# Optimization experiments

Hardware: AMD Instinct MI355X
Metric: run time of the kernel (lower is better)

The kernel has to match this reference:

```python
import jax, jax.numpy as jnp
import numpy as np

B, T, C, H, D = 2048, 64, 64, 8, 64  # batch, block_size, n_embed, num_heads, head_size


def setup_inputs() -> dict:
    key = jax.random.key(0)
    ks = jax.random.split(key, 6)
    s = C ** -0.5  # approx torch Linear init scale
    x = jax.random.normal(ks[0], (B, T, C), dtype=jnp.float32)
    Wq = jax.random.uniform(ks[1], (H, C, D), jnp.float32, -s, s)  # per-head query weights (in, out)
    Wk = jax.random.uniform(ks[2], (H, C, D), jnp.float32, -s, s)
    Wv = jax.random.uniform(ks[3], (H, C, D), jnp.float32, -s, s)
    sp = (H * D) ** -0.5
    Wproj = jax.random.uniform(ks[4], (H * D, C), jnp.float32, -sp, sp)  # proj weight (in, out)
    bproj = jax.random.uniform(ks[5], (C,), jnp.float32, -sp, sp)
    return {"x": x, "Wq": Wq, "Wk": Wk, "Wv": Wv, "Wproj": Wproj, "bproj": bproj}


def reference(x, Wq, Wk, Wv, Wproj, bproj):
    # per-head projections, vectorized over heads (original loops over Head modules)
    q = jnp.einsum('btc,hcd->bhtd', x, Wq)
    k = jnp.einsum('btc,hcd->bhtd', x, Wk)
    v = jnp.einsum('btc,hcd->bhtd', x, Wv)
    scores = jnp.einsum('bhtd,bhsd->bhts', q, k) * (D ** -0.5)  # [B,H,T,T]
    causal = jnp.tril(jnp.ones((T, T), dtype=bool))
    scores = jnp.where(causal, scores, jnp.float32(-jnp.inf))
    wei = jax.nn.softmax(scores, axis=-1)  # dropout = identity in eval mode
    out = jnp.einsum('bhts,bhsd->bhtd', wei, v)
    out = out.transpose(0, 2, 1, 3).reshape(B, T, H * D)  # concat heads on last dim
    out = out @ Wproj + bproj  # output projection (dropout = identity in eval)
    return out
```

## Files before the change

### kernel.cpp

```cpp
#include <hip/hip_runtime.h>

typedef __bf16 bf16x8 __attribute__((ext_vector_type(8)));
typedef float f32x4 __attribute__((ext_vector_type(4)));
typedef unsigned short u16x4 __attribute__((ext_vector_type(4)));
typedef unsigned int u32x4 __attribute__((ext_vector_type(4)));

#define LDA 72

__device__ __forceinline__ unsigned short f2bf(float f) {
  __bf16 b = (__bf16)f;
  return __builtin_bit_cast(unsigned short, b);
}

__device__ __forceinline__ u16x4 pack4(f32x4 v) {
  u16x4 r;
  r[0] = f2bf(v[0]); r[1] = f2bf(v[1]); r[2] = f2bf(v[2]); r[3] = f2bf(v[3]);
  return r;
}

__device__ __forceinline__ bf16x8 frag8(const unsigned short* p) {
  typedef unsigned short u16x8v __attribute__((ext_vector_type(8)));
  return __builtin_bit_cast(bf16x8, *reinterpret_cast<const u16x8v*>(p));
}

#define MFMA(a, b, c) __builtin_amdgcn_mfma_f32_16x16x32_bf16(a, b, c, 0, 0, 0)

__device__ __forceinline__ void cfrag2bfrag(const f32x4 v[4], bf16x8 out[2]) {
  unsigned O[4][2];
  #pragma unroll
  for (int si = 0; si < 4; ++si) {
    u16x4 p = pack4(v[si]);
    O[si][0] = (unsigned)p[0] | ((unsigned)p[1] << 16);
    O[si][1] = (unsigned)p[2] | ((unsigned)p[3] << 16);
  }
  unsigned H[2][2][2];
  #pragma unroll
  for (int s1 = 0; s1 < 2; ++s1)
    #pragma unroll
    for (int d = 0; d < 2; ++d) {
      auto r = __builtin_amdgcn_permlane32_swap(O[2 * s1][d], O[2 * s1 + 1][d], false, false);
      H[s1][0][d] = r[0];
      H[s1][1][d] = r[1];
    }
  #pragma unroll
  for (int e1 = 0; e1 < 2; ++e1) {
    auto r0 = __builtin_amdgcn_permlane16_swap(H[e1][0][0], H[e1][1][0], false, false);
    auto r1 = __builtin_amdgcn_permlane16_swap(H[e1][0][1], H[e1][1][1], false, false);
    u32x4 f;
    f[0] = r0[0]; f[1] = r1[0]; f[2] = r0[1]; f[3] = r1[1];
    out[e1] = __builtin_bit_cast(bf16x8, f);
  }
}

__global__ __launch_bounds__(256) void fuse_pack(
    const float* __restrict__ Wq, const float* __restrict__ Wk,
    const float* __restrict__ Wv, const float* __restrict__ Wp,
    unsigned short* __restrict__ wf) {
  __shared__ float A[64 * 65];
  __shared__ float B[64 * 65];
  const int blk = blockIdx.x;
  const int t = blk >> 3, h = blk & 7;
  const int tid = threadIdx.x;
  const float* Asrc = (t ? Wv : Wq) + h * 4096;
  const float* Bsrc = (t ? Wp : Wk) + h * 4096;
  for (int i = tid; i < 4096; i += 256) {
    A[(i >> 6) * 65 + (i & 63)] = Asrc[i];
    B[(i >> 6) * 65 + (i & 63)] = Bsrc[i];
  }
  __syncthreads();
  unsigned short* dst = wf + blk * 4096;
  for (int o = 0; o < 16; ++o) {
    int idx = o * 256 + tid;
    int k = idx >> 6, n = idx & 63;
    float s = 0.f;
    if (t == 0) {
      for (int d = 0; d < 64; ++d) s += A[k * 65 + d] * B[n * 65 + d];
      s *= 0.18033688f;
    } else {
      for (int d = 0; d < 64; ++d) s += A[k * 65 + d] * B[d * 65 + n];
    }
    int kk = k >> 5, i = k & 7, lg = (k >> 3) & 3, si = n >> 4, l15 = n & 15;
    dst[((kk * 4 + si) * 64 + lg * 16 + l15) * 8 + i] = f2bf(s);
  }
}

__global__ __launch_bounds__(256, 2) void mha_fwd(
    const float* __restrict__ x, const unsigned short* __restrict__ wf,
    const float* __restrict__ bproj, float* __restrict__ out) {
  __shared__ __attribute__((aligned(16))) unsigned short Xs[4][64 * LDA];

  const int tid  = threadIdx.x;
  const int lane = tid & 63;
  const int w    = tid >> 6;
  const int l15  = lane & 15;
  const int g    = lane >> 4;
  const int kcol = 8 * g;

  const float* xb = x + (size_t)blockIdx.x * 16384;
  #pragma unroll
  for (int it = 0; it < 16; ++it) {
    int idx = it * 1024 + tid * 4;
    float4 v = *reinterpret_cast<const float4*>(xb + idx);
    f32x4 vv = {v.x, v.y, v.z, v.w};
    int bt = idx >> 12, rem = idx & 4095;
    *reinterpret_cast<u16x4*>(&Xs[bt][(rem >> 6) * LDA + (rem & 63)]) = pack4(vv);
  }
  __syncthreads();

  bf16x8 xf[2][4];
  #pragma unroll
  for (int cc = 0; cc < 2; ++cc)
    #pragma unroll
    for (int t = 0; t < 4; ++t)
      xf[cc][t] = frag8(&Xs[w][(t * 16 + l15) * LDA + cc * 32 + kcol]);

  f32x4 oacc[4][4];
  #pragma unroll
  for (int nt = 0; nt < 4; ++nt) {
    float bias = bproj[nt * 16 + l15];
    f32x4 bv = {bias, bias, bias, bias};
    #pragma unroll
    for (int mt = 0; mt < 4; ++mt) oacc[mt][nt] = bv;
  }

  for (int h = 0; h < 8; ++h) {
    const unsigned short* mf = wf + h * 4096;
    const unsigned short* nf = wf + 32768 + h * 4096;

    bf16x8 gB[2][4];
    #pragma unroll
    for (int mt = 0; mt < 4; ++mt) {
      f32x4 gc[4] = {};
      #pragma unroll
      for (int kk = 0; kk < 2; ++kk)
        #pragma unroll
        for (int ct = 0; ct < 4; ++ct)
          gc[ct] = MFMA(frag8(&mf[(kk * 4 + ct) * 512 + lane * 8]), xf[kk][mt], gc[ct]);
      bf16x8 o2[2];
      cfrag2bfrag(gc, o2);
      gB[0][mt] = o2[0]; gB[1][mt] = o2[1];
    }

    bf16x8 pA[2][4];
    #pragma unroll
    for (int mt = 0; mt < 4; ++mt) {
      f32x4 sc[4] = {};
      #pragma unroll
      for (int cc = 0; cc < 2; ++cc)
        #pragma unroll
        for (int st = 0; st < 4; ++st)
          sc[st] = MFMA(xf[cc][st], gB[cc][mt], sc[st]);
      const int m = mt * 16 + l15;
      float sum = 0.f;
      #pragma unroll
      for (int st = 0; st < 4; ++st)
        #pragma unroll
        for (int r = 0; r < 4; ++r) {
          int s = st * 16 + 4 * g + r;
          float e = (s <= m) ? exp2f(sc[st][r]) : 0.f;
          sc[st][r] = e;
          sum += e;
        }
      sum += __shfl_xor(sum, 16);
      sum += __shfl_xor(sum, 32);
      float rinv = __builtin_amdgcn_rcpf(sum);
      #pragma unroll
      for (int st = 0; st < 4; ++st) sc[st] *= rinv;
      bf16x8 o2[2];
      cfrag2bfrag(sc, o2);
      pA[0][mt] = o2[0]; pA[1][mt] = o2[1];
    }

    bf16x8 zB[2][4];
    #pragma unroll
    for (int nt = 0; nt < 4; ++nt) {
      bf16x8 nf0 = frag8(&nf[(0 * 4 + nt) * 512 + lane * 8]);
      bf16x8 nf1 = frag8(&nf[(1 * 4 + nt) * 512 + lane * 8]);
      f32x4 zc[4] = {};
      #pragma unroll
      for (int st = 0; st < 4; ++st) {
        zc[st] = MFMA(xf[0][st], nf0, zc[st]);
        zc[st] = MFMA(xf[1][st], nf1, zc[st]);
      }
      bf16x8 o2[2];
      cfrag2bfrag(zc, o2);
      zB[0][nt] = o2[0]; zB[1][nt] = o2[1];
    }

    #pragma unroll
    for (int mt = 0; mt < 4; ++mt)
      #pragma unroll
      for (int nt = 0; nt < 4; ++nt) {
        oacc[mt][nt] = MFMA(pA[0][mt], zB[0][nt], oacc[mt][nt]);
        oacc[mt][nt] = MFMA(pA[1][mt], zB[1][nt], oacc[mt][nt]);
      }
  }

  float* ob = out + ((size_t)blockIdx.x * 4 + w) * 4096;
  #pragma unroll
  for (int mt = 0; mt < 4; ++mt)
    #pragma unroll
    for (int r = 0; r < 4; ++r) {
      float* orow = ob + (mt * 16 + 4 * g + r) * 64;
      #pragma unroll
      for (int nt = 0; nt < 4; ++nt)
        orow[nt * 16 + l15] = oacc[mt][nt][r];
    }
}

extern "C" void kernel_launch(void* const* d_in, const int* in_sizes, int n_in,
                              void* d_out, int out_size, void* d_ws, size_t ws_size,
                              hipStream_t stream) {
  const float* x  = (const float*)d_in[0];
  const float* Wq = (const float*)d_in[1];
  const float* Wk = (const float*)d_in[2];
  const float* Wv = (const float*)d_in[3];
  const float* Wp = (const float*)d_in[4];
  const float* bp = (const float*)d_in[5];
  unsigned short* wf = (unsigned short*)d_ws;

  fuse_pack<<<dim3(16), dim3(256), 0, stream>>>(Wq, Wk, Wv, Wp, wf);
  mha_fwd<<<dim3(512), dim3(256), 0, stream>>>(x, wf, bp, (float*)d_out);
}
```

Measured before the change: 61.43 us.

## Split each batch across two waves with balanced causal row tiles and skip masked MFMAs

Each wave now owns two of the four query row tiles of one batch element instead of a whole batch element. The pairs are (0,3) and (1,2) so causal work is balanced between the two waves. Score MFMAs, exp work and P·V MFMAs for fully masked key tiles are skipped at compile time via templated tile indices. The grid doubles, launch bounds ask for 4 blocks per CU, and register pressure per wave drops. The cost is that the Z (V·Wproj) fragment is now recomputed by both waves sharing a batch element.

```diff
diff --git a/kernel.cpp b/kernel.cpp
--- a/kernel.cpp
+++ b/kernel.cpp
@@ -6,6 +6,8 @@
 typedef unsigned int u32x4 __attribute__((ext_vector_type(4)));
 
 #define LDA 72
+
+template <int N> struct Int { static constexpr int value = N; };
 
 __device__ __forceinline__ unsigned short f2bf(float f) {
   __bf16 b = (__bf16)f;
@@ -84,26 +86,28 @@
   }
 }
 
-__global__ __launch_bounds__(256, 2) void mha_fwd(
+__global__ __launch_bounds__(256, 4) void mha_fwd(
     const float* __restrict__ x, const unsigned short* __restrict__ wf,
     const float* __restrict__ bproj, float* __restrict__ out) {
-  __shared__ __attribute__((aligned(16))) unsigned short Xs[4][64 * LDA];
+  __shared__ __attribute__((aligned(16))) unsigned short Xs[2][64 * LDA];
 
   const int tid  = threadIdx.x;
   const int lane = tid & 63;
   const int w    = tid >> 6;
+  const int bt   = w >> 1;
+  const int mg   = w & 1;
   const int l15  = lane & 15;
   const int g    = lane >> 4;
   const int kcol = 8 * g;
 
-  const float* xb = x + (size_t)blockIdx.x * 16384;
-  #pragma unroll
-  for (int it = 0; it < 16; ++it) {
+  const float* xb = x + (size_t)blockIdx.x * 8192;
+  #pragma unroll
+  for (int it = 0; it < 8; ++it) {
     int idx = it * 1024 + tid * 4;
     float4 v = *reinterpret_cast<const float4*>(xb + idx);
     f32x4 vv = {v.x, v.y, v.z, v.w};
-    int bt = idx >> 12, rem = idx & 4095;
-    *reinterpret_cast<u16x4*>(&Xs[bt][(rem >> 6) * LDA + (rem & 63)]) = pack4(vv);
+    int sb = idx >> 12, rem = idx & 4095;
+    *reinterpret_cast<u16x4*>(&Xs[sb][(rem >> 6) * LDA + (rem & 63)]) = pack4(vv);
   }
   __syncthreads();
 
@@ -112,100 +116,112 @@
   for (int cc = 0; cc < 2; ++cc)
     #pragma unroll
     for (int t = 0; t < 4; ++t)
-      xf[cc][t] = frag8(&Xs[w][(t * 16 + l15) * LDA + cc * 32 + kcol]);
-
-  f32x4 oacc[4][4];
+      xf[cc][t] = frag8(&Xs[bt][(t * 16 + l15) * LDA + cc * 32 + kcol]);
+
+  f32x4 oacc[2][4];
   #pragma unroll
   for (int nt = 0; nt < 4; ++nt) {
     float bias = bproj[nt * 16 + l15];
     f32x4 bv = {bias, bias, bias, bias};
-    #pragma unroll
-    for (int mt = 0; mt < 4; ++mt) oacc[mt][nt] = bv;
-  }
-
+    oacc[0][nt] = bv;
+    oacc[1][nt] = bv;
+  }
+
+  #pragma unroll 1
   for (int h = 0; h < 8; ++h) {
     const unsigned short* mf = wf + h * 4096;
     const unsigned short* nf = wf + 32768 + h * 4096;
 
-    bf16x8 gB[2][4];
-    #pragma unroll
-    for (int mt = 0; mt < 4; ++mt) {
-      f32x4 gc[4] = {};
-      #pragma unroll
-      for (int kk = 0; kk < 2; ++kk)
-        #pragma unroll
-        for (int ct = 0; ct < 4; ++ct)
-          gc[ct] = MFMA(frag8(&mf[(kk * 4 + ct) * 512 + lane * 8]), xf[kk][mt], gc[ct]);
-      bf16x8 o2[2];
-      cfrag2bfrag(gc, o2);
-      gB[0][mt] = o2[0]; gB[1][mt] = o2[1];
-    }
-
-    bf16x8 pA[2][4];
-    #pragma unroll
-    for (int mt = 0; mt < 4; ++mt) {
-      f32x4 sc[4] = {};
-      #pragma unroll
-      for (int cc = 0; cc < 2; ++cc)
+    auto head_body = [&](auto MT0C, auto MT1C) {
+      constexpr int MT0 = decltype(MT0C)::value;
+      constexpr int MT1 = decltype(MT1C)::value;
+      bf16x8 pA[2][2];
+
+      auto gs = [&](auto MTC, int lmt) {
+        constexpr int MT = decltype(MTC)::value;
+        f32x4 gc[4] = {};
+        #pragma unroll
+        for (int kk = 0; kk < 2; ++kk)
+          #pragma unroll
+          for (int ct = 0; ct < 4; ++ct)
+            gc[ct] = MFMA(frag8(&mf[(kk * 4 + ct) * 512 + lane * 8]), xf[kk][MT], gc[ct]);
+        bf16x8 gB[2];
+        cfrag2bfrag(gc, gB);
+
+        f32x4 sc[4] = {};
+        #pragma unroll
+        for (int cc = 0; cc < 2; ++cc)
+          #pragma unroll
+          for (int st = 0; st < 4; ++st)
+            if (st <= MT)
+              sc[st] = MFMA(xf[cc][st], gB[cc], sc[st]);
+
+        const int m = MT * 16 + l15;
+        float sum = 0.f;
+        #pragma unroll
+        for (int st = 0; st < 4; ++st) {
+          if (st < MT) {
+            #pragma unroll
+            for (int r = 0; r < 4; ++r) { float e = exp2f(sc[st][r]); sc[st][r] = e; sum += e; }
+          } else if (st == MT) {
+            #pragma unroll
+            for (int r = 0; r < 4; ++r) {
+              int s = st * 16 + 4 * g + r;
+              float e = (s <= m) ? exp2f(sc[st][r]) : 0.f;
+              sc[st][r] = e; sum += e;
+            }
+          }
+        }
+        sum += __shfl_xor(sum, 16);
+        sum += __shfl_xor(sum, 32);
+        float rinv = __builtin_amdgcn_rcpf(sum);
         #pragma unroll
         for (int st = 0; st < 4; ++st)
-          sc[st] = MFMA(xf[cc][st], gB[cc][mt], sc[st]);
-      const int m = mt * 16 + l15;
-      float sum = 0.f;
-      #pragma unroll
-      for (int st = 0; st < 4; ++st)
-        #pragma unroll
-        for (int r = 0; r < 4; ++r) {
-          int s = st * 16 + 4 * g + r;
-          float e = (s <= m) ? exp2f(sc[st][r]) : 0.f;
-          sc[st][r] = e;
-          sum += e;
-        }
-      sum += __shfl_xor(sum, 16);
-      sum += __shfl_xor(sum, 32);
-      float rinv = __builtin_amdgcn_rcpf(sum);
-      #pragma unroll
-      for (int st = 0; st < 4; ++st) sc[st] *= rinv;
-      bf16x8 o2[2];
-      cfrag2bfrag(sc, o2);
-      pA[0][mt] = o2[0]; pA[1][mt] = o2[1];
-    }
-
-    bf16x8 zB[2][4];
-    #pragma unroll
-    for (int nt = 0; nt < 4; ++nt) {
-      bf16x8 nf0 = frag8(&nf[(0 * 4 + nt) * 512 + lane * 8]);
-      bf16x8 nf1 = frag8(&nf[(1 * 4 + nt) * 512 + lane * 8]);
-      f32x4 zc[4] = {};
-      #pragma unroll
-      for (int st = 0; st < 4; ++st) {
-        zc[st] = MFMA(xf[0][st], nf0, zc[st]);
-        zc[st] = MFMA(xf[1][st], nf1, zc[st]);
-      }
-      bf16x8 o2[2];
-      cfrag2bfrag(zc, o2);
-      zB[0][nt] = o2[0]; zB[1][nt] = o2[1];
-    }
-
-    #pragma unroll
-    for (int mt = 0; mt < 4; ++mt)
+          if (st <= MT) sc[st] *= rinv;
+        bf16x8 o2[2];
+        cfrag2bfrag(sc, o2);
+        pA[0][lmt] = o2[0]; pA[1][lmt] = o2[1];
+      };
+      gs(Int<MT0>{}, 0);
+      gs(Int<MT1>{}, 1);
+
       #pragma unroll
       for (int nt = 0; nt < 4; ++nt) {
-        oacc[mt][nt] = MFMA(pA[0][mt], zB[0][nt], oacc[mt][nt]);
-        oacc[mt][nt] = MFMA(pA[1][mt], zB[1][nt], oacc[mt][nt]);
+        bf16x8 nf0 = frag8(&nf[nt * 512 + lane * 8]);
+        bf16x8 nf1 = frag8(&nf[(4 + nt) * 512 + lane * 8]);
+        f32x4 zc[4] = {};
+        #pragma unroll
+        for (int st = 0; st < 4; ++st) {
+          zc[st] = MFMA(xf[0][st], nf0, zc[st]);
+          zc[st] = MFMA(xf[1][st], nf1, zc[st]);
+        }
+        bf16x8 zB[2];
+        cfrag2bfrag(zc, zB);
+        oacc[0][nt] = MFMA(pA[0][0], zB[0], oacc[0][nt]);
+        if (MT0 >= 2) oacc[0][nt] = MFMA(pA[1][0], zB[1], oacc[0][nt]);
+        oacc[1][nt] = MFMA(pA[0][1], zB[0], oacc[1][nt]);
+        if (MT1 >= 2) oacc[1][nt] = MFMA(pA[1][1], zB[1], oacc[1][nt]);
       }
-  }
-
-  float* ob = out + ((size_t)blockIdx.x * 4 + w) * 4096;
-  #pragma unroll
-  for (int mt = 0; mt < 4; ++mt)
+    };
+
+    if (mg == 0) head_body(Int<0>{}, Int<3>{});
+    else         head_body(Int<1>{}, Int<2>{});
+  }
+
+  const int mtv0 = mg ? 1 : 0;
+  const int mtv1 = mg ? 2 : 3;
+  float* ob = out + ((size_t)blockIdx.x * 2 + bt) * 4096;
+  #pragma unroll
+  for (int lmt = 0; lmt < 2; ++lmt) {
+    int mt = lmt ? mtv1 : mtv0;
     #pragma unroll
     for (int r = 0; r < 4; ++r) {
       float* orow = ob + (mt * 16 + 4 * g + r) * 64;
       #pragma unroll
       for (int nt = 0; nt < 4; ++nt)
-        orow[nt * 16 + l15] = oacc[mt][nt][r];
+        orow[nt * 16 + l15] = oacc[lmt][nt][r];
     }
+  }
 }
 
 extern "C" void kernel_launch(void* const* d_in, const int* in_sizes, int n_in,
@@ -220,5 +236,5 @@
   unsigned short* wf = (unsigned short*)d_ws;
 
   fuse_pack<<<dim3(16), dim3(256), 0, stream>>>(Wq, Wk, Wv, Wp, wf);
-  mha_fwd<<<dim3(512), dim3(256), 0, stream>>>(x, wf, bp, (float*)d_out);
-}
+  mha_fwd<<<dim3(1024), dim3(256), 0, stream>>>(x, wf, bp, (float*)d_out);
+}
```

New measurement: 61.28 us. About the same (-0.3%).
